# Performance work log

Measured on AMD Instinct MI355X. Metric: run time of the kernel, lower is better.

Reference implementation:

```python
import jax, jax.numpy as jnp
import numpy as np

N, D, D_QK, D_V = 8192, 1024, 256, 256
SCALE = float(np.sqrt(D_QK))  # NB: module MULTIPLIES by sqrt(D_qk)


def setup_inputs() -> dict:
    key = jax.random.key(0)
    kx, kq, kk, kv = jax.random.split(key, 4)
    x = jax.random.normal(kx, (N, D), dtype=jnp.float32)
    # torch nn.Linear(D, D_out, bias=False) weight has shape [D_out, D]
    s = 1.0 / np.sqrt(D)
    Wq = jax.random.uniform(kq, (D_QK, D), jnp.float32, -s, s)
    Wk = jax.random.uniform(kk, (D_QK, D), jnp.float32, -s, s)
    Wv = jax.random.uniform(kv, (D_V, D), jnp.float32, -s, s)
    return {"x": x, "Wq": Wq, "Wk": Wk, "Wv": Wv}


def reference(x, Wq, Wk, Wv):
    q = x @ Wq.T            # [N, D_qk]
    k = x @ Wk.T            # [N, D_qk]
    v = x @ Wv.T            # [N, D_v]
    scores = SCALE * (q @ k.T)          # [N, N] — faithful: multiply by sqrt(D_qk)
    attn = jax.nn.softmax(scores, axis=-1)
    return attn @ v                      # [N, D_v]
```

## Files before the change

kernel.cpp:

```cpp
#include <hip/hip_runtime.h>
#include <hip/hip_bf16.h>


typedef __attribute__((ext_vector_type(8))) short short8;
typedef __attribute__((ext_vector_type(4))) float f32x4;
typedef __attribute__((ext_vector_type(4))) unsigned int u32x4;

#define MFMA16(a, b, c) __builtin_amdgcn_mfma_f32_16x16x32_bf16((a), (b), (c), 0, 0, 0)

__device__ __forceinline__ unsigned short f2bf(float f) {
    unsigned int u = __builtin_bit_cast(unsigned int, f);
    u += 0x7fffu + ((u >> 16) & 1u);
    return (unsigned short)(u >> 16);
}
__device__ __forceinline__ float bf2f(unsigned short h) {
    unsigned int u = ((unsigned int)h) << 16;
    return __builtin_bit_cast(float, u);
}
__device__ __forceinline__ unsigned int cvtpk(float a, float b) {
    unsigned int r;
    asm("v_cvt_pk_bf16_f32 %0, %1, %2" : "=v"(r) : "v"(a), "v"(b));
    return r;
}
__device__ __forceinline__ void gl16(const unsigned short* g, unsigned short* l) {
    __builtin_amdgcn_global_load_lds(
        (const __attribute__((address_space(1))) unsigned int*)g,
        (__attribute__((address_space(3))) unsigned int*)l,
        16, 0, 0);
}

__global__ void convert_x_kernel(const float* __restrict__ x,
                                 unsigned short* __restrict__ xhi,
                                 unsigned short* __restrict__ xlo) {
    int i = blockIdx.x * blockDim.x + threadIdx.x;
    float4 v = reinterpret_cast<const float4*>(x)[i];
    float f[4] = {v.x, v.y, v.z, v.w};
    ushort4 hi, lo;
    unsigned short th[4], tl[4];
#pragma unroll
    for (int j = 0; j < 4; ++j) {
        th[j] = f2bf(f[j]);
        tl[j] = f2bf(f[j] - bf2f(th[j]));
    }
    hi.x = th[0]; hi.y = th[1]; hi.z = th[2]; hi.w = th[3];
    lo.x = tl[0]; lo.y = tl[1]; lo.z = tl[2]; lo.w = tl[3];
    reinterpret_cast<ushort4*>(xhi)[i] = hi;
    reinterpret_cast<ushort4*>(xlo)[i] = lo;
}

__global__ void convert_w_kernel(const float* __restrict__ Wq,
                                 const float* __restrict__ Wk,
                                 const float* __restrict__ Wv,
                                 unsigned short* __restrict__ Whi,
                                 unsigned short* __restrict__ Wlo) {
    const float* W = (blockIdx.y == 0) ? Wq : (blockIdx.y == 1) ? Wk : Wv;
    int i = blockIdx.x * blockDim.x + threadIdx.x;
    float4 v = reinterpret_cast<const float4*>(W)[i];
    float f[4] = {v.x, v.y, v.z, v.w};
    ushort4 hi, lo;
    unsigned short th[4], tl[4];
#pragma unroll
    for (int j = 0; j < 4; ++j) {
        th[j] = f2bf(f[j]);
        tl[j] = f2bf(f[j] - bf2f(th[j]));
    }
    hi.x = th[0]; hi.y = th[1]; hi.z = th[2]; hi.w = th[3];
    lo.x = tl[0]; lo.y = tl[1]; lo.z = tl[2]; lo.w = tl[3];
    size_t off = (size_t)blockIdx.y * 65536 + i;
    reinterpret_cast<ushort4*>(Whi)[off] = hi;
    reinterpret_cast<ushort4*>(Wlo)[off] = lo;
}

__launch_bounds__(256, 4)
__global__ void proj_kernel(const unsigned short* __restrict__ xhi,
                            const unsigned short* __restrict__ xlo,
                            const unsigned short* __restrict__ Whi,
                            const unsigned short* __restrict__ Wlo,
                            unsigned short* __restrict__ Qhi, unsigned short* __restrict__ Qlo,
                            unsigned short* __restrict__ Khi, unsigned short* __restrict__ Klo,
                            unsigned short* __restrict__ VT) {
    __shared__ __align__(16) unsigned short xh[64 * 64], xl[64 * 64];
    __shared__ __align__(16) unsigned short wh[64 * 64], wl[64 * 64];
    const int t = threadIdx.x;
    const int mtile = blockIdx.x;
    const int y = blockIdx.y;
    const int w = y >> 2, nt = y & 3;
    const int mb = mtile * 64, nb = nt * 64;
    const unsigned short* WhiW = Whi + (size_t)w * 262144;
    const unsigned short* WloW = Wlo + (size_t)w * 262144;
    const int wid = t >> 6, lane = t & 63, lr = lane & 15, lg = lane >> 4;

    int soff[2], ldst[2];
#pragma unroll
    for (int i = 0; i < 2; ++i) {
        int s = t + i * 256;
        int row = s >> 3, c = (s & 7) ^ (row & 7);
        soff[i] = row * 1024 + c * 8;
        ldst[i] = s * 8;
    }

    const f32x4 fzero = {0.f, 0.f, 0.f, 0.f};
    f32x4 acc[4];
#pragma unroll
    for (int i = 0; i < 4; ++i) acc[i] = fzero;

    for (int ks = 0; ks < 16; ++ks) {
        const int k0 = ks * 64;
#pragma unroll
        for (int i = 0; i < 2; ++i) {
            gl16(xhi + (size_t)mb * 1024 + k0 + soff[i], xh + ldst[i]);
            gl16(xlo + (size_t)mb * 1024 + k0 + soff[i], xl + ldst[i]);
            gl16(WhiW + (size_t)nb * 1024 + k0 + soff[i], wh + ldst[i]);
            gl16(WloW + (size_t)nb * 1024 + k0 + soff[i], wl + ldst[i]);
        }
        asm volatile("s_waitcnt vmcnt(0)" ::: "memory");
        __syncthreads();
        {
            const int arow = wid * 16 + lr;
            short8 ah[2], al[2];
#pragma unroll
            for (int ko = 0; ko < 2; ++ko) {
                int aidx = arow * 64 + (((ko * 4 + lg) ^ (arow & 7)) << 3);
                ah[ko] = *reinterpret_cast<const short8*>(&xh[aidx]);
                al[ko] = *reinterpret_cast<const short8*>(&xl[aidx]);
            }
#pragma unroll
            for (int ct = 0; ct < 4; ++ct) {
                const int brow = ct * 16 + lr;
#pragma unroll
                for (int ko = 0; ko < 2; ++ko) {
                    int bidx = brow * 64 + (((ko * 4 + lg) ^ (brow & 7)) << 3);
                    short8 bh = *reinterpret_cast<const short8*>(&wh[bidx]);
                    short8 bl = *reinterpret_cast<const short8*>(&wl[bidx]);
                    acc[ct] = MFMA16(ah[ko], bh, acc[ct]);
                    acc[ct] = MFMA16(ah[ko], bl, acc[ct]);
                    acc[ct] = MFMA16(al[ko], bh, acc[ct]);
                }
            }
        }
        __syncthreads();
    }
    const int rbase = mb + wid * 16 + lg * 4;
#pragma unroll
    for (int ct = 0; ct < 4; ++ct) {
        int col = nb + ct * 16 + lr;
        if (w == 2) {
            ushort4 v4;
            v4.x = f2bf(acc[ct][0]); v4.y = f2bf(acc[ct][1]);
            v4.z = f2bf(acc[ct][2]); v4.w = f2bf(acc[ct][3]);
            *reinterpret_cast<ushort4*>(VT + (size_t)col * 8192 + rbase) = v4;
        } else {
            unsigned short* Hi = (w == 0) ? Qhi : Khi;
            unsigned short* Lo = (w == 0) ? Qlo : Klo;
            const float scale = (w == 0) ? 16.0f : 1.0f;
#pragma unroll
            for (int j = 0; j < 4; ++j) {
                float v = acc[ct][j] * scale;
                unsigned short h = f2bf(v);
                unsigned short lo = f2bf(v - bf2f(h));
                Hi[(size_t)(rbase + j) * 256 + col] = h;
                Lo[(size_t)(rbase + j) * 256 + col] = lo;
            }
        }
    }
}

__launch_bounds__(256, 2)
__global__ void flash_kernel(const unsigned short* __restrict__ Qhi,
                             const unsigned short* __restrict__ Qlo,
                             const unsigned short* __restrict__ Khi_g,
                             const unsigned short* __restrict__ Klo_g,
                             const unsigned short* __restrict__ VT,
                             unsigned short* __restrict__ Opart,
                             float* __restrict__ Mpart, float* __restrict__ Lpart) {
    __shared__ __align__(16) unsigned short Kh[32 * 256], Kl[32 * 256];
    __shared__ __align__(16) unsigned short Vt[256 * 32];
    const int t = threadIdx.x;
    const int bid = blockIdx.x;
    const int work = (bid & 7) * 64 + (bid >> 3);
    const int split = work >> 7, mtile = work & 127;
    const int mb = mtile * 64;
    const int kv0 = split * 2048;
    const int wid = t >> 6, lane = t & 63, lr = lane & 15, lg = lane >> 4;

    const int qrow = mb + wid * 16 + lr;
    short8 qh[8], ql[8];
#pragma unroll
    for (int ko = 0; ko < 8; ++ko) {
        int g = qrow * 256 + ko * 32 + lg * 8;
        qh[ko] = *reinterpret_cast<const short8*>(Qhi + g);
        ql[ko] = *reinterpret_cast<const short8*>(Qlo + g);
    }

    int khoff[4], vtoff[4], kc[4];
#pragma unroll
    for (int i = 0; i < 4; ++i) {
        int c = wid * 4 + i;
        kc[i] = c * 512;
        int krow = c * 2 + (lane >> 5), ksl = lane & 31;
        khoff[i] = krow * 256 + ((ksl ^ (krow & 7)) << 3);
        int vrow = c * 16 + (lane >> 2), vl = lane & 3;
        vtoff[i] = vrow * 8192 + ((vl ^ (vrow & 3)) << 3);
    }

    const f32x4 fzero = {0.f, 0.f, 0.f, 0.f};
    f32x4 acc[16];
#pragma unroll
    for (int i = 0; i < 16; ++i) acc[i] = fzero;
    float m = -__builtin_inff(), lp = 0.f;
    const int xr7 = lr & 7, xr3 = lr & 3;
    const bool lgEven = (lg & 1) == 0;
    const bool lgMid = (lg == 1) || (lg == 2);

    for (int it = 0; it < 64; ++it) {
        const int kvb = kv0 + it * 32;
        const int kb = kvb << 8;
#pragma unroll
        for (int i = 0; i < 4; ++i) {
            gl16(Khi_g + kb + khoff[i], (unsigned short*)Kh + kc[i]);
            gl16(Klo_g + kb + khoff[i], (unsigned short*)Kl + kc[i]);
            gl16(VT + kvb + vtoff[i], (unsigned short*)Vt + kc[i]);
        }
        asm volatile("s_waitcnt vmcnt(0)" ::: "memory");
        __syncthreads();
        f32x4 s0 = fzero, s1 = fzero;
        __builtin_amdgcn_s_setprio(1);
#pragma unroll
        for (int ko = 0; ko < 8; ++ko) {
            int sl = (((ko * 4 + lg) ^ xr7) << 3);
            int b0 = lr * 256 + sl;
            int b1 = b0 + 4096;
            short8 bh0 = *reinterpret_cast<const short8*>(&Kh[b0]);
            short8 bl0 = *reinterpret_cast<const short8*>(&Kl[b0]);
            short8 bh1 = *reinterpret_cast<const short8*>(&Kh[b1]);
            short8 bl1 = *reinterpret_cast<const short8*>(&Kl[b1]);
            s0 = MFMA16(bh0, qh[ko], s0);
            s1 = MFMA16(bh1, qh[ko], s1);
            s0 = MFMA16(bl0, qh[ko], s0);
            s1 = MFMA16(bl1, qh[ko], s1);
            s0 = MFMA16(bh0, ql[ko], s0);
            s1 = MFMA16(bh1, ql[ko], s1);
        }
        __builtin_amdgcn_s_setprio(0);
        float mx = fmaxf(fmaxf(fmaxf(s0[0], s0[1]), fmaxf(s0[2], s0[3])),
                         fmaxf(fmaxf(s1[0], s1[1]), fmaxf(s1[2], s1[3])));
        mx = fmaxf(mx, __shfl_xor(mx, 16));
        mx = fmaxf(mx, __shfl_xor(mx, 32));
        if (!__all(mx - m <= 4.0f)) {
            float nm = fmaxf(m, mx);
            float sc = __expf(m - nm);
            lp *= sc;
            m = nm;
#pragma unroll
            for (int i = 0; i < 16; ++i) acc[i] *= sc;
        }
        float p0[4], p1[4];
#pragma unroll
        for (int j = 0; j < 4; ++j) {
            p0[j] = __expf(s0[j] - m);
            p1[j] = __expf(s1[j] - m);
        }
        lp += (p0[0] + p0[1]) + (p0[2] + p0[3]) + (p1[0] + p1[1]) + (p1[2] + p1[3]);
        unsigned int A0 = cvtpk(p0[0], p0[1]);
        unsigned int A1 = cvtpk(p0[2], p0[3]);
        unsigned int B0 = cvtpk(p1[0], p1[1]);
        unsigned int B1 = cvtpk(p1[2], p1[3]);
        unsigned int X0 = __shfl_xor(A0, 16), X1 = __shfl_xor(A1, 16);
        unsigned int Y0 = __shfl_xor(B0, 16), Y1 = __shfl_xor(B1, 16);
        unsigned int U0 = lgEven ? A0 : Y0, U1 = lgEven ? A1 : Y1;
        unsigned int U2 = lgEven ? X0 : B0, U3 = lgEven ? X1 : B1;
        unsigned int V0 = __shfl_xor(U0, 48), V1 = __shfl_xor(U1, 48);
        unsigned int V2 = __shfl_xor(U2, 48), V3 = __shfl_xor(U3, 48);
        u32x4 wv;
        wv[0] = lgMid ? V0 : U0; wv[1] = lgMid ? V1 : U1;
        wv[2] = lgMid ? V2 : U2; wv[3] = lgMid ? V3 : U3;
        short8 pa = __builtin_bit_cast(short8, wv);
        __builtin_amdgcn_s_setprio(1);
#pragma unroll
        for (int dt = 0; dt < 16; ++dt) {
            int vidx = (dt * 16 + lr) * 32 + ((lg ^ xr3) << 3);
            short8 bv = *reinterpret_cast<const short8*>(&Vt[vidx]);
            acc[dt] = MFMA16(bv, pa, acc[dt]);
        }
        __builtin_amdgcn_s_setprio(0);
        __syncthreads();
    }
    lp += __shfl_xor(lp, 16);
    lp += __shfl_xor(lp, 32);
    const int orow = mb + wid * 16 + lr;
    unsigned short* Ob = Opart + (size_t)split * 8192 * 256 + (size_t)orow * 256 + lg * 4;
#pragma unroll
    for (int dt = 0; dt < 16; ++dt) {
        unsigned int k0 = cvtpk(acc[dt][0], acc[dt][1]);
        unsigned int k1 = cvtpk(acc[dt][2], acc[dt][3]);
        *reinterpret_cast<unsigned int*>(Ob + dt * 16) = k0;
        *reinterpret_cast<unsigned int*>(Ob + dt * 16 + 2) = k1;
    }
    if (lg == 0) {
        Mpart[split * 8192 + orow] = m;
        Lpart[split * 8192 + orow] = lp;
    }
}

__global__ void combine_kernel(const unsigned short* __restrict__ Opart,
                               const float* __restrict__ Mpart,
                               const float* __restrict__ Lpart,
                               float* __restrict__ out) {
    const int row = blockIdx.x;
    const int d = threadIdx.x;
    float mm = -__builtin_inff();
#pragma unroll
    for (int s = 0; s < 4; ++s) mm = fmaxf(mm, Mpart[s * 8192 + row]);
    float num = 0.f, den = 0.f;
#pragma unroll
    for (int s = 0; s < 4; ++s) {
        float w = __expf(Mpart[s * 8192 + row] - mm);
        den += w * Lpart[s * 8192 + row];
        num += w * bf2f(Opart[((size_t)s * 8192 + row) * 256 + d]);
    }
    out[(size_t)row * 256 + d] = num / den;
}

extern "C" void kernel_launch(void* const* d_in, const int* in_sizes, int n_in,
                              void* d_out, int out_size, void* d_ws, size_t ws_size,
                              hipStream_t stream) {
    const float* x  = (const float*)d_in[0];
    const float* Wq = (const float*)d_in[1];
    const float* Wk = (const float*)d_in[2];
    const float* Wv = (const float*)d_in[3];
    float* out = (float*)d_out;

    char* ws = (char*)d_ws;
    const size_t SZ_QK = (size_t)8192 * 256 * 2;
    unsigned short* Qhi = (unsigned short*)(ws + 0 * SZ_QK);
    unsigned short* Qlo = (unsigned short*)(ws + 1 * SZ_QK);
    unsigned short* Khi = (unsigned short*)(ws + 2 * SZ_QK);
    unsigned short* Klo = (unsigned short*)(ws + 3 * SZ_QK);
    unsigned short* VT  = (unsigned short*)(ws + 4 * SZ_QK);
    float* Mpart = (float*)(ws + 5 * SZ_QK);
    float* Lpart = (float*)(ws + 5 * SZ_QK + 131072);
    char* uA = ws + 5 * SZ_QK + 262144;
    unsigned short* xhi = (unsigned short*)uA;
    unsigned short* xlo = (unsigned short*)(uA + (size_t)8192 * 1024 * 2);
    unsigned short* Whi = (unsigned short*)(uA + (size_t)2 * 8192 * 1024 * 2);
    unsigned short* Wlo = (unsigned short*)(uA + (size_t)2 * 8192 * 1024 * 2 + 3 * 262144 * 2);
    unsigned short* Opart = (unsigned short*)uA;

    convert_x_kernel<<<8192, 256, 0, stream>>>(x, xhi, xlo);
    convert_w_kernel<<<dim3(256, 3), 256, 0, stream>>>(Wq, Wk, Wv, Whi, Wlo);
    proj_kernel<<<dim3(128, 12), 256, 0, stream>>>(xhi, xlo, Whi, Wlo,
                                                   Qhi, Qlo, Khi, Klo, VT);
    flash_kernel<<<512, 256, 0, stream>>>(Qhi, Qlo, Khi, Klo, VT, Opart, Mpart, Lpart);
    combine_kernel<<<8192, 256, 0, stream>>>(Opart, Mpart, Lpart, out);
}
```

Before: 324.7 us.

## Enlarge proj and flash tiles to 128 rows, double-buffer K/V loads

The projection kernel moves to 128x128 tiles with 512 threads. The flash kernel now has each wave handle 32 query rows instead of 16, so every K/V tile loaded into LDS is reused across twice the rows. K/V loads are double-buffered so the next tile's global-to-LDS copy overlaps the current tile's compute, and the trailing barrier is dropped. The trade-off is higher register pressure (two accumulator sets) at occupancy 1, and only 256 flash blocks, which may underfill the GPU's CUs.

Result: slower. 333.8 us (+2.8%).

```diff
diff --git a/kernel.cpp b/kernel.cpp
--- a/kernel.cpp
+++ b/kernel.cpp
@@ -71,7 +71,7 @@
     reinterpret_cast<ushort4*>(Wlo)[off] = lo;
 }
 
-__launch_bounds__(256, 4)
+__launch_bounds__(512, 4)
 __global__ void proj_kernel(const unsigned short* __restrict__ xhi,
                             const unsigned short* __restrict__ xlo,
                             const unsigned short* __restrict__ Whi,
@@ -79,13 +79,13 @@
                             unsigned short* __restrict__ Qhi, unsigned short* __restrict__ Qlo,
                             unsigned short* __restrict__ Khi, unsigned short* __restrict__ Klo,
                             unsigned short* __restrict__ VT) {
-    __shared__ __align__(16) unsigned short xh[64 * 64], xl[64 * 64];
-    __shared__ __align__(16) unsigned short wh[64 * 64], wl[64 * 64];
+    __shared__ __align__(16) unsigned short xh[128 * 64], xl[128 * 64];
+    __shared__ __align__(16) unsigned short wh[128 * 64], wl[128 * 64];
     const int t = threadIdx.x;
     const int mtile = blockIdx.x;
     const int y = blockIdx.y;
-    const int w = y >> 2, nt = y & 3;
-    const int mb = mtile * 64, nb = nt * 64;
+    const int w = y >> 1, nt = y & 1;
+    const int mb = mtile * 128, nb = nt * 128;
     const unsigned short* WhiW = Whi + (size_t)w * 262144;
     const unsigned short* WloW = Wlo + (size_t)w * 262144;
     const int wid = t >> 6, lane = t & 63, lr = lane & 15, lg = lane >> 4;
@@ -93,16 +93,16 @@
     int soff[2], ldst[2];
 #pragma unroll
     for (int i = 0; i < 2; ++i) {
-        int s = t + i * 256;
+        int s = t + i * 512;
         int row = s >> 3, c = (s & 7) ^ (row & 7);
         soff[i] = row * 1024 + c * 8;
         ldst[i] = s * 8;
     }
 
     const f32x4 fzero = {0.f, 0.f, 0.f, 0.f};
-    f32x4 acc[4];
-#pragma unroll
-    for (int i = 0; i < 4; ++i) acc[i] = fzero;
+    f32x4 acc[8];
+#pragma unroll
+    for (int i = 0; i < 8; ++i) acc[i] = fzero;
 
     for (int ks = 0; ks < 16; ++ks) {
         const int k0 = ks * 64;
@@ -125,7 +125,7 @@
                 al[ko] = *reinterpret_cast<const short8*>(&xl[aidx]);
             }
 #pragma unroll
-            for (int ct = 0; ct < 4; ++ct) {
+            for (int ct = 0; ct < 8; ++ct) {
                 const int brow = ct * 16 + lr;
 #pragma unroll
                 for (int ko = 0; ko < 2; ++ko) {
@@ -142,7 +142,7 @@
     }
     const int rbase = mb + wid * 16 + lg * 4;
 #pragma unroll
-    for (int ct = 0; ct < 4; ++ct) {
+    for (int ct = 0; ct < 8; ++ct) {
         int col = nb + ct * 16 + lr;
         if (w == 2) {
             ushort4 v4;
@@ -165,7 +165,7 @@
     }
 }
 
-__launch_bounds__(256, 2)
+__launch_bounds__(256, 1)
 __global__ void flash_kernel(const unsigned short* __restrict__ Qhi,
                              const unsigned short* __restrict__ Qlo,
                              const unsigned short* __restrict__ Khi_g,
@@ -173,132 +173,183 @@
                              const unsigned short* __restrict__ VT,
                              unsigned short* __restrict__ Opart,
                              float* __restrict__ Mpart, float* __restrict__ Lpart) {
-    __shared__ __align__(16) unsigned short Kh[32 * 256], Kl[32 * 256];
-    __shared__ __align__(16) unsigned short Vt[256 * 32];
+    __shared__ __align__(16) unsigned short LB[2][24576];
     const int t = threadIdx.x;
     const int bid = blockIdx.x;
-    const int work = (bid & 7) * 64 + (bid >> 3);
-    const int split = work >> 7, mtile = work & 127;
-    const int mb = mtile * 64;
+    const int work = (bid & 7) * 32 + (bid >> 3);
+    const int split = work >> 6, mtile = work & 63;
+    const int mb = mtile * 128;
     const int kv0 = split * 2048;
     const int wid = t >> 6, lane = t & 63, lr = lane & 15, lg = lane >> 4;
 
-    const int qrow = mb + wid * 16 + lr;
-    short8 qh[8], ql[8];
+    const int qr0 = mb + wid * 32 + lr, qr1 = qr0 + 16;
+    short8 qh0[8], ql0[8], qh1[8], ql1[8];
 #pragma unroll
     for (int ko = 0; ko < 8; ++ko) {
-        int g = qrow * 256 + ko * 32 + lg * 8;
-        qh[ko] = *reinterpret_cast<const short8*>(Qhi + g);
-        ql[ko] = *reinterpret_cast<const short8*>(Qlo + g);
-    }
-
-    int khoff[4], vtoff[4], kc[4];
-#pragma unroll
-    for (int i = 0; i < 4; ++i) {
-        int c = wid * 4 + i;
-        kc[i] = c * 512;
-        int krow = c * 2 + (lane >> 5), ksl = lane & 31;
-        khoff[i] = krow * 256 + ((ksl ^ (krow & 7)) << 3);
-        int vrow = c * 16 + (lane >> 2), vl = lane & 3;
-        vtoff[i] = vrow * 8192 + ((vl ^ (vrow & 3)) << 3);
+        int g0 = qr0 * 256 + ko * 32 + lg * 8;
+        int g1 = qr1 * 256 + ko * 32 + lg * 8;
+        qh0[ko] = *reinterpret_cast<const short8*>(Qhi + g0);
+        ql0[ko] = *reinterpret_cast<const short8*>(Qlo + g0);
+        qh1[ko] = *reinterpret_cast<const short8*>(Qhi + g1);
+        ql1[ko] = *reinterpret_cast<const short8*>(Qlo + g1);
+    }
+
+    int goff[12], ldso[12], isV[12];
+    const unsigned short* gbase[12];
+#pragma unroll
+    for (int i = 0; i < 12; ++i) {
+        int u = wid * 12 + i;
+        int a = u >> 4, c = u & 15;
+        if (a < 2) {
+            int krow = c * 2 + (lane >> 5), ksl = lane & 31;
+            goff[i] = krow * 256 + ((ksl ^ (krow & 7)) << 3);
+            gbase[i] = (a == 0) ? Khi_g : Klo_g;
+            isV[i] = 0;
+            ldso[i] = a * 8192 + c * 512;
+        } else {
+            int vrow = c * 16 + (lane >> 2), vl = lane & 3;
+            goff[i] = vrow * 8192 + ((vl ^ (vrow & 3)) << 3);
+            gbase[i] = VT;
+            isV[i] = 1;
+            ldso[i] = 16384 + c * 512;
+        }
     }
 
     const f32x4 fzero = {0.f, 0.f, 0.f, 0.f};
-    f32x4 acc[16];
-#pragma unroll
-    for (int i = 0; i < 16; ++i) acc[i] = fzero;
-    float m = -__builtin_inff(), lp = 0.f;
+    f32x4 acc0[16], acc1[16];
+#pragma unroll
+    for (int i = 0; i < 16; ++i) { acc0[i] = fzero; acc1[i] = fzero; }
+    float m0 = -__builtin_inff(), m1 = -__builtin_inff(), lp0 = 0.f, lp1 = 0.f;
     const int xr7 = lr & 7, xr3 = lr & 3;
     const bool lgEven = (lg & 1) == 0;
     const bool lgMid = (lg == 1) || (lg == 2);
 
+    {
+        const int kvb = kv0, kb = kvb << 8;
+#pragma unroll
+        for (int i = 0; i < 12; ++i)
+            gl16(gbase[i] + (isV[i] ? kvb : kb) + goff[i], &LB[0][0] + ldso[i]);
+    }
+    int cur = 0;
     for (int it = 0; it < 64; ++it) {
-        const int kvb = kv0 + it * 32;
-        const int kb = kvb << 8;
-#pragma unroll
-        for (int i = 0; i < 4; ++i) {
-            gl16(Khi_g + kb + khoff[i], (unsigned short*)Kh + kc[i]);
-            gl16(Klo_g + kb + khoff[i], (unsigned short*)Kl + kc[i]);
-            gl16(VT + kvb + vtoff[i], (unsigned short*)Vt + kc[i]);
-        }
         asm volatile("s_waitcnt vmcnt(0)" ::: "memory");
         __syncthreads();
-        f32x4 s0 = fzero, s1 = fzero;
+        if (it + 1 < 64) {
+            const int kvb = kv0 + (it + 1) * 32, kb = kvb << 8;
+#pragma unroll
+            for (int i = 0; i < 12; ++i)
+                gl16(gbase[i] + (isV[i] ? kvb : kb) + goff[i], &LB[cur ^ 1][0] + ldso[i]);
+        }
+        const unsigned short* KhP = &LB[cur][0];
+        const unsigned short* KlP = KhP + 8192;
+        const unsigned short* VtP = KhP + 16384;
+        f32x4 s00 = fzero, s10 = fzero, s01 = fzero, s11 = fzero;
         __builtin_amdgcn_s_setprio(1);
 #pragma unroll
         for (int ko = 0; ko < 8; ++ko) {
             int sl = (((ko * 4 + lg) ^ xr7) << 3);
             int b0 = lr * 256 + sl;
             int b1 = b0 + 4096;
-            short8 bh0 = *reinterpret_cast<const short8*>(&Kh[b0]);
-            short8 bl0 = *reinterpret_cast<const short8*>(&Kl[b0]);
-            short8 bh1 = *reinterpret_cast<const short8*>(&Kh[b1]);
-            short8 bl1 = *reinterpret_cast<const short8*>(&Kl[b1]);
-            s0 = MFMA16(bh0, qh[ko], s0);
-            s1 = MFMA16(bh1, qh[ko], s1);
-            s0 = MFMA16(bl0, qh[ko], s0);
-            s1 = MFMA16(bl1, qh[ko], s1);
-            s0 = MFMA16(bh0, ql[ko], s0);
-            s1 = MFMA16(bh1, ql[ko], s1);
+            short8 bh0 = *reinterpret_cast<const short8*>(&KhP[b0]);
+            short8 bl0 = *reinterpret_cast<const short8*>(&KlP[b0]);
+            short8 bh1 = *reinterpret_cast<const short8*>(&KhP[b1]);
+            short8 bl1 = *reinterpret_cast<const short8*>(&KlP[b1]);
+            s00 = MFMA16(bh0, qh0[ko], s00);
+            s10 = MFMA16(bh1, qh0[ko], s10);
+            s01 = MFMA16(bh0, qh1[ko], s01);
+            s11 = MFMA16(bh1, qh1[ko], s11);
+            s00 = MFMA16(bl0, qh0[ko], s00);
+            s10 = MFMA16(bl1, qh0[ko], s10);
+            s01 = MFMA16(bl0, qh1[ko], s01);
+            s11 = MFMA16(bl1, qh1[ko], s11);
+            s00 = MFMA16(bh0, ql0[ko], s00);
+            s10 = MFMA16(bh1, ql0[ko], s10);
+            s01 = MFMA16(bh0, ql1[ko], s01);
+            s11 = MFMA16(bh1, ql1[ko], s11);
         }
         __builtin_amdgcn_s_setprio(0);
-        float mx = fmaxf(fmaxf(fmaxf(s0[0], s0[1]), fmaxf(s0[2], s0[3])),
-                         fmaxf(fmaxf(s1[0], s1[1]), fmaxf(s1[2], s1[3])));
-        mx = fmaxf(mx, __shfl_xor(mx, 16));
-        mx = fmaxf(mx, __shfl_xor(mx, 32));
-        if (!__all(mx - m <= 4.0f)) {
-            float nm = fmaxf(m, mx);
-            float sc = __expf(m - nm);
-            lp *= sc;
-            m = nm;
-#pragma unroll
-            for (int i = 0; i < 16; ++i) acc[i] *= sc;
-        }
-        float p0[4], p1[4];
+        float mx0 = fmaxf(fmaxf(fmaxf(s00[0], s00[1]), fmaxf(s00[2], s00[3])),
+                          fmaxf(fmaxf(s10[0], s10[1]), fmaxf(s10[2], s10[3])));
+        float mx1 = fmaxf(fmaxf(fmaxf(s01[0], s01[1]), fmaxf(s01[2], s01[3])),
+                          fmaxf(fmaxf(s11[0], s11[1]), fmaxf(s11[2], s11[3])));
+        mx0 = fmaxf(mx0, __shfl_xor(mx0, 16));
+        mx0 = fmaxf(mx0, __shfl_xor(mx0, 32));
+        mx1 = fmaxf(mx1, __shfl_xor(mx1, 16));
+        mx1 = fmaxf(mx1, __shfl_xor(mx1, 32));
+        if (!__all(fmaxf(mx0 - m0, mx1 - m1) <= 4.0f)) {
+            float nm0 = fmaxf(m0, mx0), nm1 = fmaxf(m1, mx1);
+            float sc0 = __expf(m0 - nm0), sc1 = __expf(m1 - nm1);
+            lp0 *= sc0; lp1 *= sc1; m0 = nm0; m1 = nm1;
+#pragma unroll
+            for (int i = 0; i < 16; ++i) { acc0[i] *= sc0; acc1[i] *= sc1; }
+        }
+        float p00[4], p10[4], p01[4], p11[4];
 #pragma unroll
         for (int j = 0; j < 4; ++j) {
-            p0[j] = __expf(s0[j] - m);
-            p1[j] = __expf(s1[j] - m);
-        }
-        lp += (p0[0] + p0[1]) + (p0[2] + p0[3]) + (p1[0] + p1[1]) + (p1[2] + p1[3]);
-        unsigned int A0 = cvtpk(p0[0], p0[1]);
-        unsigned int A1 = cvtpk(p0[2], p0[3]);
-        unsigned int B0 = cvtpk(p1[0], p1[1]);
-        unsigned int B1 = cvtpk(p1[2], p1[3]);
-        unsigned int X0 = __shfl_xor(A0, 16), X1 = __shfl_xor(A1, 16);
-        unsigned int Y0 = __shfl_xor(B0, 16), Y1 = __shfl_xor(B1, 16);
-        unsigned int U0 = lgEven ? A0 : Y0, U1 = lgEven ? A1 : Y1;
-        unsigned int U2 = lgEven ? X0 : B0, U3 = lgEven ? X1 : B1;
-        unsigned int V0 = __shfl_xor(U0, 48), V1 = __shfl_xor(U1, 48);
-        unsigned int V2 = __shfl_xor(U2, 48), V3 = __shfl_xor(U3, 48);
-        u32x4 wv;
-        wv[0] = lgMid ? V0 : U0; wv[1] = lgMid ? V1 : U1;
-        wv[2] = lgMid ? V2 : U2; wv[3] = lgMid ? V3 : U3;
-        short8 pa = __builtin_bit_cast(short8, wv);
+            p00[j] = __expf(s00[j] - m0);
+            p10[j] = __expf(s10[j] - m0);
+            p01[j] = __expf(s01[j] - m1);
+            p11[j] = __expf(s11[j] - m1);
+        }
+        lp0 += (p00[0] + p00[1]) + (p00[2] + p00[3]) + (p10[0] + p10[1]) + (p10[2] + p10[3]);
+        lp1 += (p01[0] + p01[1]) + (p01[2] + p01[3]) + (p11[0] + p11[1]) + (p11[2] + p11[3]);
+        short8 pa0, pa1;
+        {
+            unsigned int A0 = cvtpk(p00[0], p00[1]), A1 = cvtpk(p00[2], p00[3]);
+            unsigned int B0 = cvtpk(p10[0], p10[1]), B1 = cvtpk(p10[2], p10[3]);
+            unsigned int X0 = __shfl_xor(A0, 16), X1 = __shfl_xor(A1, 16);
+            unsigned int Y0 = __shfl_xor(B0, 16), Y1 = __shfl_xor(B1, 16);
+            unsigned int U0 = lgEven ? A0 : Y0, U1 = lgEven ? A1 : Y1;
+            unsigned int U2 = lgEven ? X0 : B0, U3 = lgEven ? X1 : B1;
+            unsigned int V0 = __shfl_xor(U0, 48), V1 = __shfl_xor(U1, 48);
+            unsigned int V2 = __shfl_xor(U2, 48), V3 = __shfl_xor(U3, 48);
+            u32x4 wv;
+            wv[0] = lgMid ? V0 : U0; wv[1] = lgMid ? V1 : U1;
+            wv[2] = lgMid ? V2 : U2; wv[3] = lgMid ? V3 : U3;
+            pa0 = __builtin_bit_cast(short8, wv);
+        }
+        {
+            unsigned int A0 = cvtpk(p01[0], p01[1]), A1 = cvtpk(p01[2], p01[3]);
+            unsigned int B0 = cvtpk(p11[0], p11[1]), B1 = cvtpk(p11[2], p11[3]);
+            unsigned int X0 = __shfl_xor(A0, 16), X1 = __shfl_xor(A1, 16);
+            unsigned int Y0 = __shfl_xor(B0, 16), Y1 = __shfl_xor(B1, 16);
+            unsigned int U0 = lgEven ? A0 : Y0, U1 = lgEven ? A1 : Y1;
+            unsigned int U2 = lgEven ? X0 : B0, U3 = lgEven ? X1 : B1;
+            unsigned int V0 = __shfl_xor(U0, 48), V1 = __shfl_xor(U1, 48);
+            unsigned int V2 = __shfl_xor(U2, 48), V3 = __shfl_xor(U3, 48);
+            u32x4 wv;
+            wv[0] = lgMid ? V0 : U0; wv[1] = lgMid ? V1 : U1;
+            wv[2] = lgMid ? V2 : U2; wv[3] = lgMid ? V3 : U3;
+            pa1 = __builtin_bit_cast(short8, wv);
+        }
         __builtin_amdgcn_s_setprio(1);
 #pragma unroll
         for (int dt = 0; dt < 16; ++dt) {
             int vidx = (dt * 16 + lr) * 32 + ((lg ^ xr3) << 3);
-            short8 bv = *reinterpret_cast<const short8*>(&Vt[vidx]);
-            acc[dt] = MFMA16(bv, pa, acc[dt]);
+            short8 bv = *reinterpret_cast<const short8*>(&VtP[vidx]);
+            acc0[dt] = MFMA16(bv, pa0, acc0[dt]);
+            acc1[dt] = MFMA16(bv, pa1, acc1[dt]);
         }
         __builtin_amdgcn_s_setprio(0);
-        __syncthreads();
-    }
-    lp += __shfl_xor(lp, 16);
-    lp += __shfl_xor(lp, 32);
-    const int orow = mb + wid * 16 + lr;
-    unsigned short* Ob = Opart + (size_t)split * 8192 * 256 + (size_t)orow * 256 + lg * 4;
+        cur ^= 1;
+    }
+    lp0 += __shfl_xor(lp0, 16); lp0 += __shfl_xor(lp0, 32);
+    lp1 += __shfl_xor(lp1, 16); lp1 += __shfl_xor(lp1, 32);
+    const int or0 = mb + wid * 32 + lr, or1 = or0 + 16;
+    unsigned short* Ob0 = Opart + (size_t)split * 8192 * 256 + (size_t)or0 * 256 + lg * 4;
+    unsigned short* Ob1 = Opart + (size_t)split * 8192 * 256 + (size_t)or1 * 256 + lg * 4;
 #pragma unroll
     for (int dt = 0; dt < 16; ++dt) {
-        unsigned int k0 = cvtpk(acc[dt][0], acc[dt][1]);
-        unsigned int k1 = cvtpk(acc[dt][2], acc[dt][3]);
-        *reinterpret_cast<unsigned int*>(Ob + dt * 16) = k0;
-        *reinterpret_cast<unsigned int*>(Ob + dt * 16 + 2) = k1;
+        *reinterpret_cast<unsigned int*>(Ob0 + dt * 16)     = cvtpk(acc0[dt][0], acc0[dt][1]);
+        *reinterpret_cast<unsigned int*>(Ob0 + dt * 16 + 2) = cvtpk(acc0[dt][2], acc0[dt][3]);
+        *reinterpret_cast<unsigned int*>(Ob1 + dt * 16)     = cvtpk(acc1[dt][0], acc1[dt][1]);
+        *reinterpret_cast<unsigned int*>(Ob1 + dt * 16 + 2) = cvtpk(acc1[dt][2], acc1[dt][3]);
     }
     if (lg == 0) {
-        Mpart[split * 8192 + orow] = m;
-        Lpart[split * 8192 + orow] = lp;
+        Mpart[split * 8192 + or0] = m0;
+        Lpart[split * 8192 + or0] = lp0;
+        Mpart[split * 8192 + or1] = m1;
+        Lpart[split * 8192 + or1] = lp1;
     }
 }
 
@@ -348,8 +399,8 @@
 
     convert_x_kernel<<<8192, 256, 0, stream>>>(x, xhi, xlo);
     convert_w_kernel<<<dim3(256, 3), 256, 0, stream>>>(Wq, Wk, Wv, Whi, Wlo);
-    proj_kernel<<<dim3(128, 12), 256, 0, stream>>>(xhi, xlo, Whi, Wlo,
-                                                   Qhi, Qlo, Khi, Klo, VT);
-    flash_kernel<<<512, 256, 0, stream>>>(Qhi, Qlo, Khi, Klo, VT, Opart, Mpart, Lpart);
+    proj_kernel<<<dim3(64, 6), 512, 0, stream>>>(xhi, xlo, Whi, Wlo,
+                                                 Qhi, Qlo, Khi, Klo, VT);
+    flash_kernel<<<256, 256, 0, stream>>>(Qhi, Qlo, Khi, Klo, VT, Opart, Mpart, Lpart);
     combine_kernel<<<8192, 256, 0, stream>>>(Opart, Mpart, Lpart, out);
 }
```

## Double-buffer flash K/V tiles and enlarge proj and flash tiles to 512 threads

Applied to the files above, without the earlier changes.

The flash kernel now uses 512-thread blocks over 128-row query tiles and loads K-hi, K-lo and V^T into a unified double-buffered LDS region. The next tile is prefetched while the current one is computed, and the trailing barrier is removed. The V^T layout in LDS is re-swizzled to suit the new chunking. The projection kernel doubles its tile to 128x128 with 512 threads. Together these aim to hide global-load latency and cut per-tile synchronisation, at the cost of more LDS per block, fewer blocks and possible occupancy loss.

Measured after the change: 271.1 us. 16.5% less time.

```diff
diff --git a/kernel.cpp b/kernel.cpp
--- a/kernel.cpp
+++ b/kernel.cpp
@@ -71,7 +71,7 @@
     reinterpret_cast<ushort4*>(Wlo)[off] = lo;
 }
 
-__launch_bounds__(256, 4)
+__launch_bounds__(512, 4)
 __global__ void proj_kernel(const unsigned short* __restrict__ xhi,
                             const unsigned short* __restrict__ xlo,
                             const unsigned short* __restrict__ Whi,
@@ -79,13 +79,13 @@
                             unsigned short* __restrict__ Qhi, unsigned short* __restrict__ Qlo,
                             unsigned short* __restrict__ Khi, unsigned short* __restrict__ Klo,
                             unsigned short* __restrict__ VT) {
-    __shared__ __align__(16) unsigned short xh[64 * 64], xl[64 * 64];
-    __shared__ __align__(16) unsigned short wh[64 * 64], wl[64 * 64];
+    __shared__ __align__(16) unsigned short xh[128 * 64], xl[128 * 64];
+    __shared__ __align__(16) unsigned short wh[128 * 64], wl[128 * 64];
     const int t = threadIdx.x;
     const int mtile = blockIdx.x;
     const int y = blockIdx.y;
-    const int w = y >> 2, nt = y & 3;
-    const int mb = mtile * 64, nb = nt * 64;
+    const int w = y >> 1, nt = y & 1;
+    const int mb = mtile * 128, nb = nt * 128;
     const unsigned short* WhiW = Whi + (size_t)w * 262144;
     const unsigned short* WloW = Wlo + (size_t)w * 262144;
     const int wid = t >> 6, lane = t & 63, lr = lane & 15, lg = lane >> 4;
@@ -93,16 +93,16 @@
     int soff[2], ldst[2];
 #pragma unroll
     for (int i = 0; i < 2; ++i) {
-        int s = t + i * 256;
+        int s = t + i * 512;
         int row = s >> 3, c = (s & 7) ^ (row & 7);
         soff[i] = row * 1024 + c * 8;
         ldst[i] = s * 8;
     }
 
     const f32x4 fzero = {0.f, 0.f, 0.f, 0.f};
-    f32x4 acc[4];
-#pragma unroll
-    for (int i = 0; i < 4; ++i) acc[i] = fzero;
+    f32x4 acc[8];
+#pragma unroll
+    for (int i = 0; i < 8; ++i) acc[i] = fzero;
 
     for (int ks = 0; ks < 16; ++ks) {
         const int k0 = ks * 64;
@@ -125,7 +125,7 @@
                 al[ko] = *reinterpret_cast<const short8*>(&xl[aidx]);
             }
 #pragma unroll
-            for (int ct = 0; ct < 4; ++ct) {
+            for (int ct = 0; ct < 8; ++ct) {
                 const int brow = ct * 16 + lr;
 #pragma unroll
                 for (int ko = 0; ko < 2; ++ko) {
@@ -142,7 +142,7 @@
     }
     const int rbase = mb + wid * 16 + lg * 4;
 #pragma unroll
-    for (int ct = 0; ct < 4; ++ct) {
+    for (int ct = 0; ct < 8; ++ct) {
         int col = nb + ct * 16 + lr;
         if (w == 2) {
             ushort4 v4;
@@ -165,7 +165,7 @@
     }
 }
 
-__launch_bounds__(256, 2)
+__launch_bounds__(512, 2)
 __global__ void flash_kernel(const unsigned short* __restrict__ Qhi,
                              const unsigned short* __restrict__ Qlo,
                              const unsigned short* __restrict__ Khi_g,
@@ -173,13 +173,12 @@
                              const unsigned short* __restrict__ VT,
                              unsigned short* __restrict__ Opart,
                              float* __restrict__ Mpart, float* __restrict__ Lpart) {
-    __shared__ __align__(16) unsigned short Kh[32 * 256], Kl[32 * 256];
-    __shared__ __align__(16) unsigned short Vt[256 * 32];
+    __shared__ __align__(16) unsigned short LB[2][24576];
     const int t = threadIdx.x;
     const int bid = blockIdx.x;
-    const int work = (bid & 7) * 64 + (bid >> 3);
-    const int split = work >> 7, mtile = work & 127;
-    const int mb = mtile * 64;
+    const int work = (bid & 7) * 32 + (bid >> 3);
+    const int split = work >> 6, mtile = work & 63;
+    const int mb = mtile * 128;
     const int kv0 = split * 2048;
     const int wid = t >> 6, lane = t & 63, lr = lane & 15, lg = lane >> 4;
 
@@ -192,15 +191,26 @@
         ql[ko] = *reinterpret_cast<const short8*>(Qlo + g);
     }
 
-    int khoff[4], vtoff[4], kc[4];
-#pragma unroll
-    for (int i = 0; i < 4; ++i) {
-        int c = wid * 4 + i;
-        kc[i] = c * 512;
-        int krow = c * 2 + (lane >> 5), ksl = lane & 31;
-        khoff[i] = krow * 256 + ((ksl ^ (krow & 7)) << 3);
-        int vrow = c * 16 + (lane >> 2), vl = lane & 3;
-        vtoff[i] = vrow * 8192 + ((vl ^ (vrow & 3)) << 3);
+    int go[6], lo_[6], isv[6];
+    const unsigned short* gb[6];
+#pragma unroll
+    for (int i = 0; i < 6; ++i) {
+        int chunk = wid * 6 + i;
+        lo_[i] = chunk * 512;
+        if (chunk < 32) {
+            int cc = chunk & 15;
+            int krow = cc * 2 + (lane >> 5);
+            go[i] = krow * 256 + (((lane & 31) ^ (krow & 7)) << 3);
+            gb[i] = (chunk < 16) ? Khi_g : Klo_g;
+            isv[i] = 0;
+        } else {
+            int cc = chunk - 32;
+            int d = cc * 16 + 2 * (lane >> 3) + ((lane & 7) >> 2);
+            int csrc = (lane & 3) ^ ((lane >> 3) & 3);
+            go[i] = d * 8192 + csrc * 8;
+            gb[i] = VT;
+            isv[i] = 1;
+        }
     }
 
     const f32x4 fzero = {0.f, 0.f, 0.f, 0.f};
@@ -208,21 +218,29 @@
 #pragma unroll
     for (int i = 0; i < 16; ++i) acc[i] = fzero;
     float m = -__builtin_inff(), lp = 0.f;
-    const int xr7 = lr & 7, xr3 = lr & 3;
+    const int xr7 = lr & 7;
     const bool lgEven = (lg & 1) == 0;
     const bool lgMid = (lg == 1) || (lg == 2);
 
+    {
+        const int kvb = kv0, kb = kvb << 8;
+#pragma unroll
+        for (int i = 0; i < 6; ++i)
+            gl16(gb[i] + (isv[i] ? kvb : kb) + go[i], &LB[0][0] + lo_[i]);
+    }
+    int cur = 0;
     for (int it = 0; it < 64; ++it) {
-        const int kvb = kv0 + it * 32;
-        const int kb = kvb << 8;
-#pragma unroll
-        for (int i = 0; i < 4; ++i) {
-            gl16(Khi_g + kb + khoff[i], (unsigned short*)Kh + kc[i]);
-            gl16(Klo_g + kb + khoff[i], (unsigned short*)Kl + kc[i]);
-            gl16(VT + kvb + vtoff[i], (unsigned short*)Vt + kc[i]);
-        }
         asm volatile("s_waitcnt vmcnt(0)" ::: "memory");
         __syncthreads();
+        if (it + 1 < 64) {
+            const int kvb = kv0 + (it + 1) * 32, kb = kvb << 8;
+#pragma unroll
+            for (int i = 0; i < 6; ++i)
+                gl16(gb[i] + (isv[i] ? kvb : kb) + go[i], &LB[cur ^ 1][0] + lo_[i]);
+        }
+        const unsigned short* KhP = &LB[cur][0];
+        const unsigned short* KlP = KhP + 8192;
+        const unsigned short* VtP = KhP + 16384;
         f32x4 s0 = fzero, s1 = fzero;
         __builtin_amdgcn_s_setprio(1);
 #pragma unroll
@@ -230,10 +248,10 @@
             int sl = (((ko * 4 + lg) ^ xr7) << 3);
             int b0 = lr * 256 + sl;
             int b1 = b0 + 4096;
-            short8 bh0 = *reinterpret_cast<const short8*>(&Kh[b0]);
-            short8 bl0 = *reinterpret_cast<const short8*>(&Kl[b0]);
-            short8 bh1 = *reinterpret_cast<const short8*>(&Kh[b1]);
-            short8 bl1 = *reinterpret_cast<const short8*>(&Kl[b1]);
+            short8 bh0 = *reinterpret_cast<const short8*>(&KhP[b0]);
+            short8 bl0 = *reinterpret_cast<const short8*>(&KlP[b0]);
+            short8 bh1 = *reinterpret_cast<const short8*>(&KhP[b1]);
+            short8 bl1 = *reinterpret_cast<const short8*>(&KlP[b1]);
             s0 = MFMA16(bh0, qh[ko], s0);
             s1 = MFMA16(bh1, qh[ko], s1);
             s0 = MFMA16(bl0, qh[ko], s0);
@@ -261,10 +279,8 @@
             p1[j] = __expf(s1[j] - m);
         }
         lp += (p0[0] + p0[1]) + (p0[2] + p0[3]) + (p1[0] + p1[1]) + (p1[2] + p1[3]);
-        unsigned int A0 = cvtpk(p0[0], p0[1]);
-        unsigned int A1 = cvtpk(p0[2], p0[3]);
-        unsigned int B0 = cvtpk(p1[0], p1[1]);
-        unsigned int B1 = cvtpk(p1[2], p1[3]);
+        unsigned int A0 = cvtpk(p0[0], p0[1]), A1 = cvtpk(p0[2], p0[3]);
+        unsigned int B0 = cvtpk(p1[0], p1[1]), B1 = cvtpk(p1[2], p1[3]);
         unsigned int X0 = __shfl_xor(A0, 16), X1 = __shfl_xor(A1, 16);
         unsigned int Y0 = __shfl_xor(B0, 16), Y1 = __shfl_xor(B1, 16);
         unsigned int U0 = lgEven ? A0 : Y0, U1 = lgEven ? A1 : Y1;
@@ -278,12 +294,13 @@
         __builtin_amdgcn_s_setprio(1);
 #pragma unroll
         for (int dt = 0; dt < 16; ++dt) {
-            int vidx = (dt * 16 + lr) * 32 + ((lg ^ xr3) << 3);
-            short8 bv = *reinterpret_cast<const short8*>(&Vt[vidx]);
+            int vidx = (dt * 8 + (lr >> 1)) * 64 + ((lr & 1) << 5)
+                     + ((lg ^ ((lr >> 1) & 3)) << 3);
+            short8 bv = *reinterpret_cast<const short8*>(&VtP[vidx]);
             acc[dt] = MFMA16(bv, pa, acc[dt]);
         }
         __builtin_amdgcn_s_setprio(0);
-        __syncthreads();
+        cur ^= 1;
     }
     lp += __shfl_xor(lp, 16);
     lp += __shfl_xor(lp, 32);
@@ -291,10 +308,8 @@
     unsigned short* Ob = Opart + (size_t)split * 8192 * 256 + (size_t)orow * 256 + lg * 4;
 #pragma unroll
     for (int dt = 0; dt < 16; ++dt) {
-        unsigned int k0 = cvtpk(acc[dt][0], acc[dt][1]);
-        unsigned int k1 = cvtpk(acc[dt][2], acc[dt][3]);
-        *reinterpret_cast<unsigned int*>(Ob + dt * 16) = k0;
-        *reinterpret_cast<unsigned int*>(Ob + dt * 16 + 2) = k1;
+        *reinterpret_cast<unsigned int*>(Ob + dt * 16)     = cvtpk(acc[dt][0], acc[dt][1]);
+        *reinterpret_cast<unsigned int*>(Ob + dt * 16 + 2) = cvtpk(acc[dt][2], acc[dt][3]);
     }
     if (lg == 0) {
         Mpart[split * 8192 + orow] = m;
@@ -348,8 +363,8 @@
 
     convert_x_kernel<<<8192, 256, 0, stream>>>(x, xhi, xlo);
     convert_w_kernel<<<dim3(256, 3), 256, 0, stream>>>(Wq, Wk, Wv, Whi, Wlo);
-    proj_kernel<<<dim3(128, 12), 256, 0, stream>>>(xhi, xlo, Whi, Wlo,
-                                                   Qhi, Qlo, Khi, Klo, VT);
-    flash_kernel<<<512, 256, 0, stream>>>(Qhi, Qlo, Khi, Klo, VT, Opart, Mpart, Lpart);
+    proj_kernel<<<dim3(64, 6), 512, 0, stream>>>(xhi, xlo, Whi, Wlo,
+                                                 Qhi, Qlo, Khi, Klo, VT);
+    flash_kernel<<<256, 512, 0, stream>>>(Qhi, Qlo, Khi, Klo, VT, Opart, Mpart, Lpart);
     combine_kernel<<<8192, 256, 0, stream>>>(Opart, Mpart, Lpart, out);
 }
```
